# Kernel optimization log

Measured on AMD Instinct MI355X. Metric: run time of the kernel, lower is better.

The kernel has to match this reference:

```python
import jax, jax.numpy as jnp
import numpy as np

N = 50000
E = 1600000
IN_CH = 34
HID = 64
OUT = 64
NEG_SLOPE = 0.2


def _gat_layer(x, src, dst, W, a_src, a_dst, bias, heads, out_ch, concat):
    n = x.shape[0]
    xw = (x @ W).reshape(n, heads, out_ch)                      # [N,H,C]
    al_src = jnp.sum(xw * a_src[None], axis=-1)                  # [N,H]
    al_dst = jnp.sum(xw * a_dst[None], axis=-1)                  # [N,H]
    e = jax.nn.leaky_relu(al_src[src] + al_dst[dst], NEG_SLOPE)  # [E,H]
    # segment softmax over incoming edges of each dst node (self-loops ensure non-empty)
    m = jax.ops.segment_max(e, dst, num_segments=n)              # [N,H]
    ex = jnp.exp(e - m[dst])
    denom = jax.ops.segment_sum(ex, dst, num_segments=n)         # [N,H]
    alpha = ex / denom[dst]                                      # [E,H]
    msg = xw[src] * alpha[:, :, None]                            # [E,H,C]
    out = jax.ops.segment_sum(msg, dst, num_segments=n)          # [N,H,C]
    if concat:
        out = out.reshape(n, heads * out_ch)
    else:
        out = out.mean(axis=1)
    return out + bias


def setup_inputs() -> dict:
    key = jax.random.key(0)
    ks = jax.random.split(key, 12)
    x = jax.random.normal(ks[0], (N, IN_CH), dtype=jnp.float32)
    edge_index = jax.random.randint(ks[1], (2, E), 0, N, dtype=jnp.int64)
    # layer 1: heads=2, concat -> 128
    W1 = jax.random.normal(ks[2], (IN_CH, 2 * HID), dtype=jnp.float32) * 0.1
    a_src1 = jax.random.normal(ks[3], (2, HID), dtype=jnp.float32) * 0.1
    a_dst1 = jax.random.normal(ks[4], (2, HID), dtype=jnp.float32) * 0.1
    b1 = jnp.zeros((2 * HID,), dtype=jnp.float32)
    # layer 2: heads=1, mean
    W2 = jax.random.normal(ks[5], (2 * HID, OUT), dtype=jnp.float32) * 0.1
    a_src2 = jax.random.normal(ks[6], (1, OUT), dtype=jnp.float32) * 0.1
    a_dst2 = jax.random.normal(ks[7], (1, OUT), dtype=jnp.float32) * 0.1
    b2 = jnp.zeros((OUT,), dtype=jnp.float32)
    return {"x": x, "edge_index": edge_index, "W1": W1, "a_src1": a_src1,
            "a_dst1": a_dst1, "b1": b1, "W2": W2, "a_src2": a_src2,
            "a_dst2": a_dst2, "b2": b2}


def reference(x, edge_index, W1, a_src1, a_dst1, b1, W2, a_src2, a_dst2, b2):
    n = x.shape[0]
    loops = jnp.arange(n, dtype=edge_index.dtype)
    src = jnp.concatenate([edge_index[0], loops])  # PyG GATConv add_self_loops=True
    dst = jnp.concatenate([edge_index[1], loops])
    h = _gat_layer(x, src, dst, W1, a_src1, a_dst1, b1, heads=2, out_ch=HID, concat=True)
    h = jax.nn.relu(h)
    out = _gat_layer(h, src, dst, W2, a_src2, a_dst2, b2, heads=1, out_ch=OUT, concat=False)
    return out
```

## Files before the change

kernel.cpp:

```cpp
#include <hip/hip_runtime.h>
#include <math.h>

#define N_NODES 50000
#define E_EDGES 1600000
#define IN_CH   34
#define NEG     0.2f
#define NB      196
#define CAP     10000

static __device__ __forceinline__ unsigned short f2bf(float f) {
    unsigned int u = __float_as_uint(f);
    u += 0x7fffu + ((u >> 16) & 1u);
    return (unsigned short)(u >> 16);
}
static __device__ __forceinline__ float bflo(unsigned int u) {
    return __uint_as_float(u << 16);
}
static __device__ __forceinline__ float bfhi(unsigned int u) {
    return __uint_as_float(u & 0xffff0000u);
}
static __device__ __forceinline__ float lrelu_exp(float e) {
    return expf(e > 0.f ? e : NEG * e);
}

static __device__ __forceinline__ int scan256_excl(int v, int* wsum) {
    const int lane = threadIdx.x & 63, wv = threadIdx.x >> 6;
    int x = v;
    #pragma unroll
    for (int off = 1; off < 64; off <<= 1) {
        int y = __shfl_up(x, off);
        if (lane >= off) x += y;
    }
    if (lane == 63) wsum[wv] = x;
    __syncthreads();
    if (threadIdx.x < 4) {
        int s = wsum[threadIdx.x];
        #pragma unroll
        for (int off = 1; off < 4; off <<= 1) {
            int y = __shfl_up(s, off);
            if ((int)threadIdx.x >= off) s += y;
        }
        wsum[threadIdx.x] = s;
    }
    __syncthreads();
    const int woff = wv ? wsum[wv - 1] : 0;
    return woff + x - v;
}

__global__ __launch_bounds__(256) void k_init(int* __restrict__ gcur)
{
    const int t = threadIdx.x;
    if (t < NB) gcur[t] = t * CAP;
}

__global__ __launch_bounds__(256) void k_bin(
    const int* __restrict__ srcA, const int* __restrict__ dstA,
    int* __restrict__ gcur, unsigned int* __restrict__ binned)
{
    __shared__ unsigned int raw[8192];
    __shared__ unsigned int ebuf[8192];
    __shared__ int cnt[256], loff[256], lcur[256], cur[256];
    __shared__ int wsum[4];
    const int tid = threadIdx.x;
    cnt[tid] = 0;
    __syncthreads();
    const int base = blockIdx.x * 8192;
    #pragma unroll
    for (int i = 0; i < 32; ++i) {
        const int e = base + i * 256 + tid;
        if (e < E_EDGES) {
            const int d = dstA[e], s = srcA[e];
            raw[i * 256 + tid] = ((unsigned int)d << 16) | (unsigned int)s;
            atomicAdd(&cnt[d >> 8], 1);
        }
    }
    __syncthreads();
    const int v = cnt[tid];
    const int excl = scan256_excl(v, wsum);
    loff[tid] = excl;
    lcur[tid] = excl;
    cur[tid] = (tid < NB && v > 0) ? atomicAdd(&gcur[tid], v) : 0;
    __syncthreads();
    const int mE = min(8192, E_EDGES - base);
    #pragma unroll
    for (int i = 0; i < 32; ++i) {
        const int p = i * 256 + tid;
        if (p < mE) {
            const unsigned int u = raw[p];
            const int q = atomicAdd(&lcur[u >> 24], 1);
            ebuf[q] = u;
        }
    }
    __syncthreads();
    #pragma unroll
    for (int i = 0; i < 32; ++i) {
        const int p = i * 256 + tid;
        if (p < mE) {
            const unsigned int u = ebuf[p];
            const int b = (int)(u >> 24);
            binned[cur[b] + (p - loff[b])] = u;
        }
    }
}

__global__ __launch_bounds__(256) void k_fine(
    const int* __restrict__ gcur, const unsigned int* __restrict__ binned,
    int2* __restrict__ rowspan, int* __restrict__ sorted_src)
{
    __shared__ unsigned int sbin[CAP];
    __shared__ int cnt[256], lcur[256];
    __shared__ int wsum[4];
    const int tid = threadIdx.x;
    const int b = blockIdx.x;
    const int bbase = b * CAP;
    const int cntb = gcur[b] - bbase;
    cnt[tid] = 0;
    __syncthreads();
    for (int p = tid; p < cntb; p += 256) {
        const unsigned int u = binned[bbase + p];
        sbin[p] = u;
        atomicAdd(&cnt[(u >> 16) & 255], 1);
    }
    __syncthreads();
    const int v = cnt[tid];
    const int excl = scan256_excl(v, wsum);
    const int node = b * 256 + tid;
    if (node < N_NODES) rowspan[node] = make_int2(bbase + excl, bbase + excl + v);
    lcur[tid] = excl;
    __syncthreads();
    for (int p = tid; p < cntb; p += 256) {
        const unsigned int u = sbin[p];
        const int q = atomicAdd(&lcur[(u >> 16) & 255], 1);
        sorted_src[bbase + q] = (int)(u & 0xffffu);
    }
}

__global__ __launch_bounds__(256) void k_node1(
    const float* __restrict__ x, const float* __restrict__ W1,
    const float* __restrict__ a_src, const float* __restrict__ a_dst,
    unsigned short* __restrict__ xw1b,
    float* __restrict__ al_s, float* __restrict__ al_d)
{
    __shared__ float sW[IN_CH * 132];
    __shared__ float sx[32 * 35];
    __shared__ float sas[128], sad[128];
    const int tid = threadIdx.x;
    for (int i = tid; i < IN_CH * 128; i += 256) {
        int k = i >> 7, c = i & 127;
        sW[k * 132 + c] = W1[i];
    }
    if (tid < 128) { sas[tid] = a_src[tid]; sad[tid] = a_dst[tid]; }
    const int n0 = blockIdx.x * 32;
    for (int i = tid; i < 32 * IN_CH; i += 256) {
        int n = i / IN_CH, c = i - n * IN_CH;
        sx[n * 35 + c] = (n0 + n < N_NODES) ? x[n0 * IN_CH + i] : 0.f;
    }
    __syncthreads();

    const int tc = tid & 31, tn = tid >> 5;
    float acc[4][4] = {{0.f}};
    for (int k = 0; k < IN_CH; ++k) {
        const float4 wv = *reinterpret_cast<const float4*>(&sW[k * 132 + 4 * tc]);
        #pragma unroll
        for (int j = 0; j < 4; ++j) {
            const float hj = sx[(4 * tn + j) * 35 + k];
            acc[j][0] += hj * wv.x; acc[j][1] += hj * wv.y;
            acc[j][2] += hj * wv.z; acc[j][3] += hj * wv.w;
        }
    }
    #pragma unroll
    for (int j = 0; j < 4; ++j) {
        const int node = n0 + 4 * tn + j;
        float ps = 0.f, pd = 0.f;
        #pragma unroll
        for (int c = 0; c < 4; ++c) {
            ps += acc[j][c] * sas[4 * tc + c];
            pd += acc[j][c] * sad[4 * tc + c];
        }
        #pragma unroll
        for (int off = 1; off < 16; off <<= 1) {
            ps += __shfl_xor(ps, off);
            pd += __shfl_xor(pd, off);
        }
        if (node < N_NODES) {
            if ((tc & 15) == 0) {
                int h = tc >> 4;
                al_s[node * 2 + h] = ps;
                al_d[node * 2 + h] = pd;
            }
            ushort4 u;
            u.x = f2bf(acc[j][0]); u.y = f2bf(acc[j][1]);
            u.z = f2bf(acc[j][2]); u.w = f2bf(acc[j][3]);
            *reinterpret_cast<ushort4*>(&xw1b[node * 128 + 4 * tc]) = u;
        }
    }
}

__global__ __launch_bounds__(256) void k_gather1(
    const int2* __restrict__ rowspan, const int* __restrict__ sorted_src,
    const uint2* __restrict__ xw1p,
    const float* __restrict__ al_s, const float* __restrict__ al_d,
    const float* __restrict__ b1, float* __restrict__ hbuf)
{
    __shared__ float4 ebuf[4][64];
    const int wave = threadIdx.x >> 6;
    const int lane = threadIdx.x & 63;
    const int node = (blockIdx.x * 256 + threadIdx.x) >> 6;
    if (node >= N_NODES) return;
    const int2 span = rowspan[node];
    const int li = lane & 31;
    const int hsel = lane >> 5;
    const bool hd0 = (li < 16);

    const float2 ald  = *reinterpret_cast<const float2*>(&al_d[node * 2]);
    const float2 als0 = *reinterpret_cast<const float2*>(&al_s[node * 2]);
    const float w0h0 = lrelu_exp(als0.x + ald.x);
    const float w0h1 = lrelu_exp(als0.y + ald.y);

    const uint2 sv = xw1p[node * 32 + li];
    const float wself = (hsel == 0) ? (hd0 ? w0h0 : w0h1) : 0.f;
    float acc0 = wself * bflo(sv.x), acc1 = wself * bfhi(sv.x);
    float acc2 = wself * bflo(sv.y), acc3 = wself * bfhi(sv.y);
    float dv0 = 0.f, dv1 = 0.f;
    float4* eb = ebuf[wave];

    for (int base = span.x; base < span.y; base += 64) {
        const int rem = span.y - base;
        const int m = rem < 64 ? rem : 64;
        if (lane < m) {
            const int s = sorted_src[base + lane];
            const float2 als = *reinterpret_cast<const float2*>(&al_s[s * 2]);
            const float w0 = lrelu_exp(als.x + ald.x);
            const float w1 = lrelu_exp(als.y + ald.y);
            dv0 += w0; dv1 += w1;
            eb[lane] = make_float4(__int_as_float(s << 5), w0, w1, 0.f);
        } else if (lane == m && (m & 1)) {
            eb[m] = make_float4(__int_as_float(0), 0.f, 0.f, 0.f);
        }
        const int pairs = (m + 1) >> 1;
        int pr = 0;
        for (; pr + 4 <= pairs; pr += 4) {
            const float4 q0 = eb[2 * pr + 0 + hsel];
            const float4 q1 = eb[2 * pr + 2 + hsel];
            const float4 q2 = eb[2 * pr + 4 + hsel];
            const float4 q3 = eb[2 * pr + 6 + hsel];
            const uint2 v0 = xw1p[__float_as_int(q0.x) + li];
            const uint2 v1 = xw1p[__float_as_int(q1.x) + li];
            const uint2 v2 = xw1p[__float_as_int(q2.x) + li];
            const uint2 v3 = xw1p[__float_as_int(q3.x) + li];
            const float w0 = hd0 ? q0.y : q0.z;
            const float w1 = hd0 ? q1.y : q1.z;
            const float w2 = hd0 ? q2.y : q2.z;
            const float w3 = hd0 ? q3.y : q3.z;
            acc0 += w0 * bflo(v0.x); acc1 += w0 * bfhi(v0.x);
            acc2 += w0 * bflo(v0.y); acc3 += w0 * bfhi(v0.y);
            acc0 += w1 * bflo(v1.x); acc1 += w1 * bfhi(v1.x);
            acc2 += w1 * bflo(v1.y); acc3 += w1 * bfhi(v1.y);
            acc0 += w2 * bflo(v2.x); acc1 += w2 * bfhi(v2.x);
            acc2 += w2 * bflo(v2.y); acc3 += w2 * bfhi(v2.y);
            acc0 += w3 * bflo(v3.x); acc1 += w3 * bfhi(v3.x);
            acc2 += w3 * bflo(v3.y); acc3 += w3 * bfhi(v3.y);
        }
        for (; pr < pairs; ++pr) {
            const float4 q = eb[2 * pr + hsel];
            const uint2 v = xw1p[__float_as_int(q.x) + li];
            const float w = hd0 ? q.y : q.z;
            acc0 += w * bflo(v.x); acc1 += w * bfhi(v.x);
            acc2 += w * bflo(v.y); acc3 += w * bfhi(v.y);
        }
    }
    acc0 += __shfl_xor(acc0, 32); acc1 += __shfl_xor(acc1, 32);
    acc2 += __shfl_xor(acc2, 32); acc3 += __shfl_xor(acc3, 32);
    #pragma unroll
    for (int off = 32; off; off >>= 1) {
        dv0 += __shfl_xor(dv0, off);
        dv1 += __shfl_xor(dv1, off);
    }
    if (lane < 32) {
        const float den = hd0 ? (dv0 + w0h0) : (dv1 + w0h1);
        const float4 bv = *reinterpret_cast<const float4*>(&b1[4 * li]);
        float o0 = acc0 / den + bv.x, o1 = acc1 / den + bv.y;
        float o2 = acc2 / den + bv.z, o3 = acc3 / den + bv.w;
        o0 = o0 > 0.f ? o0 : 0.f; o1 = o1 > 0.f ? o1 : 0.f;
        o2 = o2 > 0.f ? o2 : 0.f; o3 = o3 > 0.f ? o3 : 0.f;
        *reinterpret_cast<float4*>(&hbuf[node * 128 + 4 * li]) =
            make_float4(o0, o1, o2, o3);
    }
}

__global__ __launch_bounds__(256) void k_node2(
    const float* __restrict__ hbuf, const float* __restrict__ W2,
    const float* __restrict__ a_src, const float* __restrict__ a_dst,
    unsigned short* __restrict__ xw2b, float* __restrict__ al_s, float* __restrict__ al_d)
{
    __shared__ float sW[128 * 64];
    __shared__ float sh[64 * 129];
    __shared__ float sas[64], sad[64];
    const int tid = threadIdx.x;
    for (int i = tid; i < 128 * 64; i += 256) sW[i] = W2[i];
    if (tid < 64) { sas[tid] = a_src[tid]; sad[tid] = a_dst[tid]; }
    const int n0 = blockIdx.x * 64;
    for (int i = tid; i < 64 * 128; i += 256) {
        int n = i >> 7, c = i & 127;
        sh[n * 129 + c] = (n0 + n < N_NODES) ? hbuf[(long)(n0 + n) * 128 + c] : 0.f;
    }
    __syncthreads();

    const int tc = tid & 15, tn = tid >> 4;
    float acc[4][4] = {{0.f}};
    for (int k = 0; k < 128; ++k) {
        const float4 wv = *reinterpret_cast<const float4*>(&sW[k * 64 + 4 * tc]);
        #pragma unroll
        for (int j = 0; j < 4; ++j) {
            const float hj = sh[(4 * tn + j) * 129 + k];
            acc[j][0] += hj * wv.x; acc[j][1] += hj * wv.y;
            acc[j][2] += hj * wv.z; acc[j][3] += hj * wv.w;
        }
    }
    #pragma unroll
    for (int j = 0; j < 4; ++j) {
        const int node = n0 + 4 * tn + j;
        float ps = 0.f, pd = 0.f;
        #pragma unroll
        for (int c = 0; c < 4; ++c) {
            ps += acc[j][c] * sas[4 * tc + c];
            pd += acc[j][c] * sad[4 * tc + c];
        }
        #pragma unroll
        for (int off = 1; off < 16; off <<= 1) {
            ps += __shfl_xor(ps, off);
            pd += __shfl_xor(pd, off);
        }
        if (node < N_NODES) {
            if (tc == 0) { al_s[node] = ps; al_d[node] = pd; }
            ushort4 u;
            u.x = f2bf(acc[j][0]); u.y = f2bf(acc[j][1]);
            u.z = f2bf(acc[j][2]); u.w = f2bf(acc[j][3]);
            *reinterpret_cast<ushort4*>(&xw2b[node * 64 + 4 * tc]) = u;
        }
    }
}

__global__ __launch_bounds__(256) void k_gather2(
    const int2* __restrict__ rowspan, const int* __restrict__ sorted_src,
    const unsigned int* __restrict__ xw2p,
    const float* __restrict__ al_s, const float* __restrict__ al_d,
    const float* __restrict__ b2, float* __restrict__ out)
{
    __shared__ float2 ebuf[4][64];
    const int wave = threadIdx.x >> 6;
    const int lane = threadIdx.x & 63;
    const int node = (blockIdx.x * 256 + threadIdx.x) >> 6;
    if (node >= N_NODES) return;
    const int2 span = rowspan[node];
    const int li = lane & 31;
    const int hsel = lane >> 5;

    const float ald = al_d[node];
    const float w0s = lrelu_exp(al_s[node] + ald);
    const unsigned int sv = xw2p[node * 32 + li];
    const float wself = (hsel == 0) ? w0s : 0.f;
    float acc0 = wself * bflo(sv), acc1 = wself * bfhi(sv);
    float dv = 0.f;
    float2* eb = ebuf[wave];

    for (int base = span.x; base < span.y; base += 64) {
        const int rem = span.y - base;
        const int m = rem < 64 ? rem : 64;
        if (lane < m) {
            const int s = sorted_src[base + lane];
            const float w = lrelu_exp(al_s[s] + ald);
            dv += w;
            eb[lane] = make_float2(__int_as_float(s << 5), w);
        } else if (lane == m && (m & 1)) {
            eb[m] = make_float2(__int_as_float(0), 0.f);
        }
        const int pairs = (m + 1) >> 1;
        int pr = 0;
        for (; pr + 4 <= pairs; pr += 4) {
            const float2 q0 = eb[2 * pr + 0 + hsel];
            const float2 q1 = eb[2 * pr + 2 + hsel];
            const float2 q2 = eb[2 * pr + 4 + hsel];
            const float2 q3 = eb[2 * pr + 6 + hsel];
            const unsigned int v0 = xw2p[__float_as_int(q0.x) + li];
            const unsigned int v1 = xw2p[__float_as_int(q1.x) + li];
            const unsigned int v2 = xw2p[__float_as_int(q2.x) + li];
            const unsigned int v3 = xw2p[__float_as_int(q3.x) + li];
            acc0 += q0.y * bflo(v0); acc1 += q0.y * bfhi(v0);
            acc0 += q1.y * bflo(v1); acc1 += q1.y * bfhi(v1);
            acc0 += q2.y * bflo(v2); acc1 += q2.y * bfhi(v2);
            acc0 += q3.y * bflo(v3); acc1 += q3.y * bfhi(v3);
        }
        for (; pr < pairs; ++pr) {
            const float2 q = eb[2 * pr + hsel];
            const unsigned int v = xw2p[__float_as_int(q.x) + li];
            acc0 += q.y * bflo(v); acc1 += q.y * bfhi(v);
        }
    }
    acc0 += __shfl_xor(acc0, 32); acc1 += __shfl_xor(acc1, 32);
    #pragma unroll
    for (int off = 32; off; off >>= 1) dv += __shfl_xor(dv, off);
    if (lane < 32) {
        const float den = dv + w0s;
        const float2 bv = *reinterpret_cast<const float2*>(&b2[2 * li]);
        *reinterpret_cast<float2*>(&out[node * 64 + 2 * li]) =
            make_float2(acc0 / den + bv.x, acc1 / den + bv.y);
    }
}

extern "C" void kernel_launch(void* const* d_in, const int* in_sizes, int n_in,
                              void* d_out, int out_size, void* d_ws, size_t ws_size,
                              hipStream_t stream)
{
    const float* x   = (const float*)d_in[0];
    const int*   ei  = (const int*)d_in[1];
    const float* W1  = (const float*)d_in[2];
    const float* as1 = (const float*)d_in[3];
    const float* ad1 = (const float*)d_in[4];
    const float* b1  = (const float*)d_in[5];
    const float* W2  = (const float*)d_in[6];
    const float* as2 = (const float*)d_in[7];
    const float* ad2 = (const float*)d_in[8];
    const float* b2  = (const float*)d_in[9];
    float* out = (float*)d_out;

    const int* srcA = ei;
    const int* dstA = ei + E_EDGES;

    char* ws = (char*)d_ws;
    int2*  rowspan    = (int2*)(ws);
    int*   sorted_src = (int*)(ws + 409600);
    int*   gcur       = (int*)(ws + 8249600);
    float* al_s1      = (float*)(ws + 8251648);
    float* al_d1      = (float*)(ws + 8651648);
    float* al_s2      = (float*)(ws + 9051648);
    float* al_d2      = (float*)(ws + 9251648);
    unsigned short* xw1b = (unsigned short*)(ws + 9451648);
    float* hbuf       = (float*)(ws + 22251648);
    unsigned int* binned = (unsigned int*)hbuf;
    unsigned short* xw2b = (unsigned short*)(ws + 47851648);

    hipLaunchKernelGGL(k_init, dim3(1), dim3(256), 0, stream, gcur);
    hipLaunchKernelGGL(k_bin, dim3((E_EDGES + 8191) / 8192), dim3(256), 0, stream,
                       srcA, dstA, gcur, binned);
    hipLaunchKernelGGL(k_fine, dim3(NB), dim3(256), 0, stream,
                       gcur, binned, rowspan, sorted_src);

    hipLaunchKernelGGL(k_node1, dim3((N_NODES + 31) / 32), dim3(256), 0, stream,
                       x, W1, as1, ad1, xw1b, al_s1, al_d1);
    hipLaunchKernelGGL(k_gather1, dim3((N_NODES + 3) / 4), dim3(256), 0, stream,
                       rowspan, sorted_src, (const uint2*)xw1b,
                       al_s1, al_d1, b1, hbuf);
    hipLaunchKernelGGL(k_node2, dim3((N_NODES + 63) / 64), dim3(256), 0, stream,
                       hbuf, W2, as2, ad2, xw2b, al_s2, al_d2);
    hipLaunchKernelGGL(k_gather2, dim3((N_NODES + 3) / 4), dim3(256), 0, stream,
                       rowspan, sorted_src, (const unsigned int*)xw2b,
                       al_s2, al_d2, b2, out);
}
```

Measured before the change: 278.4 us.

## Merge edge binning with layer-1 projection and restructure gather lane mapping

Fuses the edge coarse-binning kernel and the layer-1 node projection into one launch, with blocks branching by index, and replaces the init kernel with a memset that stores relative counts. This removes two launches and lets the independent projection overlap with binning. The layer-1 gather now gives each head a full 64-lane half-row per edge, fetching two edges per step with packed float2 math. The layer-2 gather is reworked to pair edges in shared memory, padding with the node's own row at zero weight instead of row 0. The merged kernel needs a large shared buffer sized for the binning path, which may lower occupancy for the projection blocks.

```diff
diff --git a/kernel.cpp b/kernel.cpp
--- a/kernel.cpp
+++ b/kernel.cpp
@@ -7,6 +7,8 @@
 #define NEG     0.2f
 #define NB      196
 #define CAP     10000
+
+typedef __attribute__((ext_vector_type(2))) float fv2;
 
 static __device__ __forceinline__ unsigned short f2bf(float f) {
     unsigned int u = __float_as_uint(f);
@@ -47,58 +49,117 @@
     return woff + x - v;
 }
 
-__global__ __launch_bounds__(256) void k_init(int* __restrict__ gcur)
-{
-    const int t = threadIdx.x;
-    if (t < NB) gcur[t] = t * CAP;
-}
-
-__global__ __launch_bounds__(256) void k_bin(
+__global__ __launch_bounds__(256) void k_bin_node1(
     const int* __restrict__ srcA, const int* __restrict__ dstA,
-    int* __restrict__ gcur, unsigned int* __restrict__ binned)
-{
-    __shared__ unsigned int raw[8192];
-    __shared__ unsigned int ebuf[8192];
-    __shared__ int cnt[256], loff[256], lcur[256], cur[256];
-    __shared__ int wsum[4];
+    int* __restrict__ gcur, unsigned int* __restrict__ binned,
+    const float* __restrict__ x, const float* __restrict__ W1,
+    const float* __restrict__ a_src, const float* __restrict__ a_dst,
+    unsigned short* __restrict__ xw1b,
+    float* __restrict__ al_s, float* __restrict__ al_d)
+{
+    __shared__ __align__(16) char sm[69664];
     const int tid = threadIdx.x;
-    cnt[tid] = 0;
-    __syncthreads();
-    const int base = blockIdx.x * 8192;
-    #pragma unroll
-    for (int i = 0; i < 32; ++i) {
-        const int e = base + i * 256 + tid;
-        if (e < E_EDGES) {
-            const int d = dstA[e], s = srcA[e];
-            raw[i * 256 + tid] = ((unsigned int)d << 16) | (unsigned int)s;
-            atomicAdd(&cnt[d >> 8], 1);
-        }
-    }
-    __syncthreads();
-    const int v = cnt[tid];
-    const int excl = scan256_excl(v, wsum);
-    loff[tid] = excl;
-    lcur[tid] = excl;
-    cur[tid] = (tid < NB && v > 0) ? atomicAdd(&gcur[tid], v) : 0;
-    __syncthreads();
-    const int mE = min(8192, E_EDGES - base);
-    #pragma unroll
-    for (int i = 0; i < 32; ++i) {
-        const int p = i * 256 + tid;
-        if (p < mE) {
-            const unsigned int u = raw[p];
-            const int q = atomicAdd(&lcur[u >> 24], 1);
-            ebuf[q] = u;
-        }
-    }
-    __syncthreads();
-    #pragma unroll
-    for (int i = 0; i < 32; ++i) {
-        const int p = i * 256 + tid;
-        if (p < mE) {
-            const unsigned int u = ebuf[p];
-            const int b = (int)(u >> 24);
-            binned[cur[b] + (p - loff[b])] = u;
+
+    if (blockIdx.x < NB) {
+        unsigned int* raw  = (unsigned int*)sm;
+        unsigned int* ebuf = (unsigned int*)(sm + 32768);
+        int* cnt  = (int*)(sm + 65536);
+        int* loff = (int*)(sm + 66560);
+        int* lcur = (int*)(sm + 67584);
+        int* cur  = (int*)(sm + 68608);
+        int* wsum = (int*)(sm + 69632);
+        cnt[tid] = 0;
+        __syncthreads();
+        const int base = blockIdx.x * 8192;
+        #pragma unroll
+        for (int i = 0; i < 32; ++i) {
+            const int e = base + i * 256 + tid;
+            if (e < E_EDGES) {
+                const int d = dstA[e], s = srcA[e];
+                raw[i * 256 + tid] = ((unsigned int)d << 16) | (unsigned int)s;
+                atomicAdd(&cnt[d >> 8], 1);
+            }
+        }
+        __syncthreads();
+        const int v = cnt[tid];
+        const int excl = scan256_excl(v, wsum);
+        loff[tid] = excl;
+        lcur[tid] = excl;
+        cur[tid] = (tid < NB && v > 0) ? (tid * CAP + atomicAdd(&gcur[tid], v)) : 0;
+        __syncthreads();
+        const int mE = min(8192, E_EDGES - base);
+        #pragma unroll
+        for (int i = 0; i < 32; ++i) {
+            const int p = i * 256 + tid;
+            if (p < mE) {
+                const unsigned int u = raw[p];
+                const int q = atomicAdd(&lcur[u >> 24], 1);
+                ebuf[q] = u;
+            }
+        }
+        __syncthreads();
+        #pragma unroll
+        for (int i = 0; i < 32; ++i) {
+            const int p = i * 256 + tid;
+            if (p < mE) {
+                const unsigned int u = ebuf[p];
+                const int b = (int)(u >> 24);
+                binned[cur[b] + (p - loff[b])] = u;
+            }
+        }
+    } else {
+        float* sW  = (float*)sm;
+        float* sx  = (float*)(sm + 17952);
+        float* sas = (float*)(sm + 22432);
+        float* sad = (float*)(sm + 22944);
+        for (int i = tid; i < IN_CH * 128; i += 256) {
+            int k = i >> 7, c = i & 127;
+            sW[k * 132 + c] = W1[i];
+        }
+        if (tid < 128) { sas[tid] = a_src[tid]; sad[tid] = a_dst[tid]; }
+        const int n0 = (blockIdx.x - NB) * 32;
+        for (int i = tid; i < 32 * IN_CH; i += 256) {
+            int n = i / IN_CH;
+            sx[n * 35 + (i - n * IN_CH)] = (n0 + n < N_NODES) ? x[n0 * IN_CH + i] : 0.f;
+        }
+        __syncthreads();
+
+        const int tc = tid & 31, tn = tid >> 5;
+        float acc[4][4] = {{0.f}};
+        for (int k = 0; k < IN_CH; ++k) {
+            const float4 wv = *reinterpret_cast<const float4*>(&sW[k * 132 + 4 * tc]);
+            #pragma unroll
+            for (int j = 0; j < 4; ++j) {
+                const float hj = sx[(4 * tn + j) * 35 + k];
+                acc[j][0] += hj * wv.x; acc[j][1] += hj * wv.y;
+                acc[j][2] += hj * wv.z; acc[j][3] += hj * wv.w;
+            }
+        }
+        #pragma unroll
+        for (int j = 0; j < 4; ++j) {
+            const int node = n0 + 4 * tn + j;
+            float ps = 0.f, pd = 0.f;
+            #pragma unroll
+            for (int c = 0; c < 4; ++c) {
+                ps += acc[j][c] * sas[4 * tc + c];
+                pd += acc[j][c] * sad[4 * tc + c];
+            }
+            #pragma unroll
+            for (int off = 1; off < 16; off <<= 1) {
+                ps += __shfl_xor(ps, off);
+                pd += __shfl_xor(pd, off);
+            }
+            if (node < N_NODES) {
+                if ((tc & 15) == 0) {
+                    int h = tc >> 4;
+                    al_s[node * 2 + h] = ps;
+                    al_d[node * 2 + h] = pd;
+                }
+                ushort4 u;
+                u.x = f2bf(acc[j][0]); u.y = f2bf(acc[j][1]);
+                u.z = f2bf(acc[j][2]); u.w = f2bf(acc[j][3]);
+                *reinterpret_cast<ushort4*>(&xw1b[node * 128 + 4 * tc]) = u;
+            }
         }
     }
 }
@@ -113,7 +174,7 @@
     const int tid = threadIdx.x;
     const int b = blockIdx.x;
     const int bbase = b * CAP;
-    const int cntb = gcur[b] - bbase;
+    const int cntb = gcur[b];
     cnt[tid] = 0;
     __syncthreads();
     for (int p = tid; p < cntb; p += 256) {
@@ -135,157 +196,97 @@
     }
 }
 
-__global__ __launch_bounds__(256) void k_node1(
-    const float* __restrict__ x, const float* __restrict__ W1,
-    const float* __restrict__ a_src, const float* __restrict__ a_dst,
-    unsigned short* __restrict__ xw1b,
-    float* __restrict__ al_s, float* __restrict__ al_d)
-{
-    __shared__ float sW[IN_CH * 132];
-    __shared__ float sx[32 * 35];
-    __shared__ float sas[128], sad[128];
-    const int tid = threadIdx.x;
-    for (int i = tid; i < IN_CH * 128; i += 256) {
-        int k = i >> 7, c = i & 127;
-        sW[k * 132 + c] = W1[i];
-    }
-    if (tid < 128) { sas[tid] = a_src[tid]; sad[tid] = a_dst[tid]; }
-    const int n0 = blockIdx.x * 32;
-    for (int i = tid; i < 32 * IN_CH; i += 256) {
-        int n = i / IN_CH, c = i - n * IN_CH;
-        sx[n * 35 + c] = (n0 + n < N_NODES) ? x[n0 * IN_CH + i] : 0.f;
-    }
-    __syncthreads();
-
-    const int tc = tid & 31, tn = tid >> 5;
-    float acc[4][4] = {{0.f}};
-    for (int k = 0; k < IN_CH; ++k) {
-        const float4 wv = *reinterpret_cast<const float4*>(&sW[k * 132 + 4 * tc]);
-        #pragma unroll
-        for (int j = 0; j < 4; ++j) {
-            const float hj = sx[(4 * tn + j) * 35 + k];
-            acc[j][0] += hj * wv.x; acc[j][1] += hj * wv.y;
-            acc[j][2] += hj * wv.z; acc[j][3] += hj * wv.w;
-        }
-    }
-    #pragma unroll
-    for (int j = 0; j < 4; ++j) {
-        const int node = n0 + 4 * tn + j;
-        float ps = 0.f, pd = 0.f;
-        #pragma unroll
-        for (int c = 0; c < 4; ++c) {
-            ps += acc[j][c] * sas[4 * tc + c];
-            pd += acc[j][c] * sad[4 * tc + c];
-        }
-        #pragma unroll
-        for (int off = 1; off < 16; off <<= 1) {
-            ps += __shfl_xor(ps, off);
-            pd += __shfl_xor(pd, off);
-        }
-        if (node < N_NODES) {
-            if ((tc & 15) == 0) {
-                int h = tc >> 4;
-                al_s[node * 2 + h] = ps;
-                al_d[node * 2 + h] = pd;
-            }
-            ushort4 u;
-            u.x = f2bf(acc[j][0]); u.y = f2bf(acc[j][1]);
-            u.z = f2bf(acc[j][2]); u.w = f2bf(acc[j][3]);
-            *reinterpret_cast<ushort4*>(&xw1b[node * 128 + 4 * tc]) = u;
-        }
-    }
-}
-
 __global__ __launch_bounds__(256) void k_gather1(
     const int2* __restrict__ rowspan, const int* __restrict__ sorted_src,
-    const uint2* __restrict__ xw1p,
+    const unsigned int* __restrict__ xw1u,
     const float* __restrict__ al_s, const float* __restrict__ al_d,
     const float* __restrict__ b1, float* __restrict__ hbuf)
 {
-    __shared__ float4 ebuf[4][64];
+    __shared__ float4 AB[2][4][32];
     const int wave = threadIdx.x >> 6;
     const int lane = threadIdx.x & 63;
     const int node = (blockIdx.x * 256 + threadIdx.x) >> 6;
     if (node >= N_NODES) return;
     const int2 span = rowspan[node];
-    const int li = lane & 31;
-    const int hsel = lane >> 5;
-    const bool hd0 = (li < 16);
+    const int head = lane >> 5;
 
     const float2 ald  = *reinterpret_cast<const float2*>(&al_d[node * 2]);
     const float2 als0 = *reinterpret_cast<const float2*>(&al_s[node * 2]);
     const float w0h0 = lrelu_exp(als0.x + ald.x);
     const float w0h1 = lrelu_exp(als0.y + ald.y);
-
-    const uint2 sv = xw1p[node * 32 + li];
-    const float wself = (hsel == 0) ? (hd0 ? w0h0 : w0h1) : 0.f;
-    float acc0 = wself * bflo(sv.x), acc1 = wself * bfhi(sv.x);
-    float acc2 = wself * bflo(sv.y), acc3 = wself * bfhi(sv.y);
+    const float wself = head ? w0h1 : w0h0;
+
+    const unsigned int su = xw1u[node * 64 + lane];
+    fv2 accX = { wself * bflo(su), wself * bfhi(su) };
+    fv2 accY = { 0.f, 0.f };
     float dv0 = 0.f, dv1 = 0.f;
-    float4* eb = ebuf[wave];
+    const float4* ABh = AB[head][wave];
 
     for (int base = span.x; base < span.y; base += 64) {
         const int rem = span.y - base;
         const int m = rem < 64 ? rem : 64;
+        const int mp = (m + 1) & ~1;
         if (lane < m) {
             const int s = sorted_src[base + lane];
             const float2 als = *reinterpret_cast<const float2*>(&al_s[s * 2]);
             const float w0 = lrelu_exp(als.x + ald.x);
             const float w1 = lrelu_exp(als.y + ald.y);
             dv0 += w0; dv1 += w1;
-            eb[lane] = make_float4(__int_as_float(s << 5), w0, w1, 0.f);
-        } else if (lane == m && (m & 1)) {
-            eb[m] = make_float4(__int_as_float(0), 0.f, 0.f, 0.f);
-        }
-        const int pairs = (m + 1) >> 1;
-        int pr = 0;
-        for (; pr + 4 <= pairs; pr += 4) {
-            const float4 q0 = eb[2 * pr + 0 + hsel];
-            const float4 q1 = eb[2 * pr + 2 + hsel];
-            const float4 q2 = eb[2 * pr + 4 + hsel];
-            const float4 q3 = eb[2 * pr + 6 + hsel];
-            const uint2 v0 = xw1p[__float_as_int(q0.x) + li];
-            const uint2 v1 = xw1p[__float_as_int(q1.x) + li];
-            const uint2 v2 = xw1p[__float_as_int(q2.x) + li];
-            const uint2 v3 = xw1p[__float_as_int(q3.x) + li];
-            const float w0 = hd0 ? q0.y : q0.z;
-            const float w1 = hd0 ? q1.y : q1.z;
-            const float w2 = hd0 ? q2.y : q2.z;
-            const float w3 = hd0 ? q3.y : q3.z;
-            acc0 += w0 * bflo(v0.x); acc1 += w0 * bfhi(v0.x);
-            acc2 += w0 * bflo(v0.y); acc3 += w0 * bfhi(v0.y);
-            acc0 += w1 * bflo(v1.x); acc1 += w1 * bfhi(v1.x);
-            acc2 += w1 * bflo(v1.y); acc3 += w1 * bfhi(v1.y);
-            acc0 += w2 * bflo(v2.x); acc1 += w2 * bfhi(v2.x);
-            acc2 += w2 * bflo(v2.y); acc3 += w2 * bfhi(v2.y);
-            acc0 += w3 * bflo(v3.x); acc1 += w3 * bfhi(v3.x);
-            acc2 += w3 * bflo(v3.y); acc3 += w3 * bfhi(v3.y);
-        }
-        for (; pr < pairs; ++pr) {
-            const float4 q = eb[2 * pr + hsel];
-            const uint2 v = xw1p[__float_as_int(q.x) + li];
-            const float w = hd0 ? q.y : q.z;
-            acc0 += w * bflo(v.x); acc1 += w * bfhi(v.x);
-            acc2 += w * bflo(v.y); acc3 += w * bfhi(v.y);
-        }
-    }
-    acc0 += __shfl_xor(acc0, 32); acc1 += __shfl_xor(acc1, 32);
-    acc2 += __shfl_xor(acc2, 32); acc3 += __shfl_xor(acc3, 32);
+            const float offf = __int_as_float(s << 6);
+            ((float2*)&AB[0][wave][lane >> 1])[lane & 1] = make_float2(offf, w0);
+            ((float2*)&AB[1][wave][lane >> 1])[lane & 1] = make_float2(offf, w1);
+        } else if (lane < mp) {
+            const float offf = __int_as_float(node << 6);
+            ((float2*)&AB[0][wave][lane >> 1])[lane & 1] = make_float2(offf, 0.f);
+            ((float2*)&AB[1][wave][lane >> 1])[lane & 1] = make_float2(offf, 0.f);
+        }
+        const int P = mp >> 1;
+        int p = 0;
+        for (; p + 4 <= P; p += 4) {
+            const float4 q0 = ABh[p + 0];
+            const float4 q1 = ABh[p + 1];
+            const float4 q2 = ABh[p + 2];
+            const float4 q3 = ABh[p + 3];
+            const unsigned int a0 = xw1u[__float_as_int(q0.x) + lane];
+            const unsigned int b0 = xw1u[__float_as_int(q0.z) + lane];
+            const unsigned int a1 = xw1u[__float_as_int(q1.x) + lane];
+            const unsigned int b1v = xw1u[__float_as_int(q1.z) + lane];
+            const unsigned int a2 = xw1u[__float_as_int(q2.x) + lane];
+            const unsigned int b2 = xw1u[__float_as_int(q2.z) + lane];
+            const unsigned int a3 = xw1u[__float_as_int(q3.x) + lane];
+            const unsigned int b3 = xw1u[__float_as_int(q3.z) + lane];
+            fv2 f;
+            f.x = bflo(a0); f.y = bfhi(a0); accX += f * q0.y;
+            f.x = bflo(b0); f.y = bfhi(b0); accY += f * q0.w;
+            f.x = bflo(a1); f.y = bfhi(a1); accX += f * q1.y;
+            f.x = bflo(b1v); f.y = bfhi(b1v); accY += f * q1.w;
+            f.x = bflo(a2); f.y = bfhi(a2); accX += f * q2.y;
+            f.x = bflo(b2); f.y = bfhi(b2); accY += f * q2.w;
+            f.x = bflo(a3); f.y = bfhi(a3); accX += f * q3.y;
+            f.x = bflo(b3); f.y = bfhi(b3); accY += f * q3.w;
+        }
+        for (; p < P; ++p) {
+            const float4 q = ABh[p];
+            const unsigned int a = xw1u[__float_as_int(q.x) + lane];
+            const unsigned int b = xw1u[__float_as_int(q.z) + lane];
+            fv2 f;
+            f.x = bflo(a); f.y = bfhi(a); accX += f * q.y;
+            f.x = bflo(b); f.y = bfhi(b); accY += f * q.w;
+        }
+    }
+    accX += accY;
     #pragma unroll
     for (int off = 32; off; off >>= 1) {
         dv0 += __shfl_xor(dv0, off);
         dv1 += __shfl_xor(dv1, off);
     }
-    if (lane < 32) {
-        const float den = hd0 ? (dv0 + w0h0) : (dv1 + w0h1);
-        const float4 bv = *reinterpret_cast<const float4*>(&b1[4 * li]);
-        float o0 = acc0 / den + bv.x, o1 = acc1 / den + bv.y;
-        float o2 = acc2 / den + bv.z, o3 = acc3 / den + bv.w;
-        o0 = o0 > 0.f ? o0 : 0.f; o1 = o1 > 0.f ? o1 : 0.f;
-        o2 = o2 > 0.f ? o2 : 0.f; o3 = o3 > 0.f ? o3 : 0.f;
-        *reinterpret_cast<float4*>(&hbuf[node * 128 + 4 * li]) =
-            make_float4(o0, o1, o2, o3);
-    }
+    const float den = head ? (dv1 + w0h1) : (dv0 + w0h0);
+    const float2 bv = *reinterpret_cast<const float2*>(&b1[2 * lane]);
+    float o0 = accX.x / den + bv.x;
+    float o1 = accX.y / den + bv.y;
+    o0 = o0 > 0.f ? o0 : 0.f;
+    o1 = o1 > 0.f ? o1 : 0.f;
+    *reinterpret_cast<float2*>(&hbuf[node * 128 + 2 * lane]) = make_float2(o0, o1);
 }
 
 __global__ __launch_bounds__(256) void k_node2(
@@ -343,68 +344,73 @@
 
 __global__ __launch_bounds__(256) void k_gather2(
     const int2* __restrict__ rowspan, const int* __restrict__ sorted_src,
-    const unsigned int* __restrict__ xw2p,
+    const unsigned int* __restrict__ xw2u,
     const float* __restrict__ al_s, const float* __restrict__ al_d,
     const float* __restrict__ b2, float* __restrict__ out)
 {
-    __shared__ float2 ebuf[4][64];
+    __shared__ float4 AB[4][32];
     const int wave = threadIdx.x >> 6;
     const int lane = threadIdx.x & 63;
     const int node = (blockIdx.x * 256 + threadIdx.x) >> 6;
     if (node >= N_NODES) return;
     const int2 span = rowspan[node];
-    const int li = lane & 31;
-    const int hsel = lane >> 5;
+    const int li = lane & 31, hsel = lane >> 5;
 
     const float ald = al_d[node];
     const float w0s = lrelu_exp(al_s[node] + ald);
-    const unsigned int sv = xw2p[node * 32 + li];
-    const float wself = (hsel == 0) ? w0s : 0.f;
-    float acc0 = wself * bflo(sv), acc1 = wself * bfhi(sv);
+    const unsigned int su = xw2u[node * 32 + li];
+    const float wself = hsel ? 0.f : w0s;
+    fv2 acc = { wself * bflo(su), wself * bfhi(su) };
     float dv = 0.f;
-    float2* eb = ebuf[wave];
+    const float4* ABw = AB[wave];
 
     for (int base = span.x; base < span.y; base += 64) {
         const int rem = span.y - base;
         const int m = rem < 64 ? rem : 64;
+        const int mp = (m + 3) & ~3;
         if (lane < m) {
             const int s = sorted_src[base + lane];
             const float w = lrelu_exp(al_s[s] + ald);
             dv += w;
-            eb[lane] = make_float2(__int_as_float(s << 5), w);
-        } else if (lane == m && (m & 1)) {
-            eb[m] = make_float2(__int_as_float(0), 0.f);
-        }
-        const int pairs = (m + 1) >> 1;
-        int pr = 0;
-        for (; pr + 4 <= pairs; pr += 4) {
-            const float2 q0 = eb[2 * pr + 0 + hsel];
-            const float2 q1 = eb[2 * pr + 2 + hsel];
-            const float2 q2 = eb[2 * pr + 4 + hsel];
-            const float2 q3 = eb[2 * pr + 6 + hsel];
-            const unsigned int v0 = xw2p[__float_as_int(q0.x) + li];
-            const unsigned int v1 = xw2p[__float_as_int(q1.x) + li];
-            const unsigned int v2 = xw2p[__float_as_int(q2.x) + li];
-            const unsigned int v3 = xw2p[__float_as_int(q3.x) + li];
-            acc0 += q0.y * bflo(v0); acc1 += q0.y * bfhi(v0);
-            acc0 += q1.y * bflo(v1); acc1 += q1.y * bfhi(v1);
-            acc0 += q2.y * bflo(v2); acc1 += q2.y * bfhi(v2);
-            acc0 += q3.y * bflo(v3); acc1 += q3.y * bfhi(v3);
-        }
-        for (; pr < pairs; ++pr) {
-            const float2 q = eb[2 * pr + hsel];
-            const unsigned int v = xw2p[__float_as_int(q.x) + li];
-            acc0 += q.y * bflo(v); acc1 += q.y * bfhi(v);
-        }
-    }
-    acc0 += __shfl_xor(acc0, 32); acc1 += __shfl_xor(acc1, 32);
+            ((float2*)&AB[wave][lane >> 1])[lane & 1] =
+                make_float2(__int_as_float(s << 5), w);
+        } else if (lane < mp) {
+            ((float2*)&AB[wave][lane >> 1])[lane & 1] =
+                make_float2(__int_as_float(node << 5), 0.f);
+        }
+        const int P = mp >> 1;
+        int p = hsel;
+        for (; p + 2 < P; p += 4) {
+            const float4 qA = ABw[p];
+            const float4 qB = ABw[p + 2];
+            const unsigned int aA = xw2u[__float_as_int(qA.x) + li];
+            const unsigned int bA = xw2u[__float_as_int(qA.z) + li];
+            const unsigned int aB = xw2u[__float_as_int(qB.x) + li];
+            const unsigned int bB = xw2u[__float_as_int(qB.z) + li];
+            fv2 f;
+            f.x = bflo(aA); f.y = bfhi(aA); acc += f * qA.y;
+            f.x = bflo(bA); f.y = bfhi(bA); acc += f * qA.w;
+            f.x = bflo(aB); f.y = bfhi(aB); acc += f * qB.y;
+            f.x = bflo(bB); f.y = bfhi(bB); acc += f * qB.w;
+        }
+        for (; p < P; p += 2) {
+            const float4 q = ABw[p];
+            const unsigned int a = xw2u[__float_as_int(q.x) + li];
+            const unsigned int b = xw2u[__float_as_int(q.z) + li];
+            fv2 f;
+            f.x = bflo(a); f.y = bfhi(a); acc += f * q.y;
+            f.x = bflo(b); f.y = bfhi(b); acc += f * q.w;
+        }
+    }
+    acc.x += __shfl_xor(acc.x, 32);
+    acc.y += __shfl_xor(acc.y, 32);
     #pragma unroll
     for (int off = 32; off; off >>= 1) dv += __shfl_xor(dv, off);
     if (lane < 32) {
         const float den = dv + w0s;
         const float2 bv = *reinterpret_cast<const float2*>(&b2[2 * li]);
         *reinterpret_cast<float2*>(&out[node * 64 + 2 * li]) =
-            make_float2(acc0 / den + bv.x, acc1 / den + bv.y);
+            make_float2(acc.x / den + bv.x, acc.y / den + bv.y);
     }
 }
 
@@ -440,16 +446,14 @@
     unsigned int* binned = (unsigned int*)hbuf;
     unsigned short* xw2b = (unsigned short*)(ws + 47851648);
 
-    hipLaunchKernelGGL(k_init, dim3(1), dim3(256), 0, stream, gcur);
-    hipLaunchKernelGGL(k_bin, dim3((E_EDGES + 8191) / 8192), dim3(256), 0, stream,
-                       srcA, dstA, gcur, binned);
+    hipMemsetAsync(gcur, 0, NB * sizeof(int), stream);
+    hipLaunchKernelGGL(k_bin_node1, dim3(NB + (N_NODES + 31) / 32), dim3(256), 0, stream,
+                       srcA, dstA, gcur, binned,
+                       x, W1, as1, ad1, xw1b, al_s1, al_d1);
     hipLaunchKernelGGL(k_fine, dim3(NB), dim3(256), 0, stream,
                        gcur, binned, rowspan, sorted_src);
-
-    hipLaunchKernelGGL(k_node1, dim3((N_NODES + 31) / 32), dim3(256), 0, stream,
-                       x, W1, as1, ad1, xw1b, al_s1, al_d1);
     hipLaunchKernelGGL(k_gather1, dim3((N_NODES + 3) / 4), dim3(256), 0, stream,
-                       rowspan, sorted_src, (const uint2*)xw1b,
+                       rowspan, sorted_src, (const unsigned int*)xw1b,
                        al_s1, al_d1, b1, hbuf);
     hipLaunchKernelGGL(k_node2, dim3((N_NODES + 63) / 64), dim3(256), 0, stream,
                        hbuf, W2, as2, ad2, xw2b, al_s2, al_d2);
```

After: 268.2 us. 1.04x faster.
